# Kernel optimization log

Measured on AMD Instinct MI355X. Metric: run time of the kernel, lower is better.

## Reference

```python
import jax, jax.numpy as jnp
import numpy as np

DIMS = [1, 16, 32, 64, 128, 64, 32, 1]  # linear chain dims, LN+ReLU after first 6 linears
EPS = 1e-5  # torch LayerNorm default


def _ln(x, g, b):
    m = jnp.mean(x, axis=-1, keepdims=True)
    v = jnp.var(x, axis=-1, keepdims=True)  # biased var, matches torch LayerNorm
    return (x - m) * jax.lax.rsqrt(v + EPS) * g + b


def setup_inputs() -> dict:
    key = jax.random.key(0)
    N = 1_048_576
    keys = jax.random.split(key, 1 + 7 * 2)
    inp = {"x": jax.random.normal(keys[0], (N, 1), dtype=jnp.float32)}
    for i in range(7):
        fan_in, fan_out = DIMS[i], DIMS[i + 1]
        bound = 1.0 / np.sqrt(fan_in)
        inp[f"W{i}"] = jax.random.uniform(keys[1 + 2 * i], (fan_in, fan_out), jnp.float32, -bound, bound)
        inp[f"b{i}"] = jax.random.uniform(keys[2 + 2 * i], (fan_out,), jnp.float32, -bound, bound)
    for i in range(6):  # LayerNorm affine params (init: gamma=1, beta=0)
        inp[f"g{i}"] = jnp.ones((DIMS[i + 1],), jnp.float32)
        inp[f"be{i}"] = jnp.zeros((DIMS[i + 1],), jnp.float32)
    return inp


def reference(x, W0, W1, W2, W3, W4, W5, W6,
              b0, b1, b2, b3, b4, b5, b6,
              g0, g1, g2, g3, g4, g5,
              be0, be1, be2, be3, be4, be5):
    Ws = [W0, W1, W2, W3, W4, W5, W6]
    bs = [b0, b1, b2, b3, b4, b5, b6]
    gs = [g0, g1, g2, g3, g4, g5]
    bes = [be0, be1, be2, be3, be4, be5]
    h = x
    for i in range(7):
        h = h @ Ws[i] + bs[i]
        if i < 6:
            h = jax.nn.relu(_ln(h, gs[i], bes[i]))
    return h
```

## Files before the change

kernel.cpp:

```cpp
#include <hip/hip_runtime.h>
#include <math.h>

#define EPS_LN 1e-5f
#define TPTS 32768
#define BT 256
#define NBLK 256

constexpr int WS_CNT  = 0;
constexpr int WS_PART = 64;
constexpr int WS_MMF  = 640;
constexpr size_t WS_TABLE_OFF = 4096;

struct Params {
  const float *W0,*b0,*W1,*b1,*W2,*b2,*W3,*b3,*W4,*b4,*W5,*b5,*W6,*b6;
  const float *g0,*be0,*g1,*be1,*g2,*be2,*g3,*be3,*g4,*be4,*g5,*be5;
};

constexpr int O_W0 = 0;      constexpr int O_B0 = 16;
constexpr int O_W1 = 32;     constexpr int O_B1 = 544;
constexpr int O_W2 = 576;    constexpr int O_B2 = 2624;
constexpr int O_W3 = 2688;   constexpr int O_B3 = 10880;
constexpr int O_W4 = 11008;  constexpr int O_B4 = 19200;
constexpr int O_W5 = 19264;  constexpr int O_B5 = 21312;
constexpr int O_W6 = 21344;  constexpr int O_B6 = 21376;
constexpr int O_G0 = 21380;  constexpr int O_BE0 = 21396;
constexpr int O_G1 = 21412;  constexpr int O_BE1 = 21444;
constexpr int O_G2 = 21476;  constexpr int O_BE2 = 21540;
constexpr int O_G3 = 21604;  constexpr int O_BE3 = 21732;
constexpr int O_G4 = 21860;  constexpr int O_BE4 = 21924;
constexpr int O_G5 = 21988;  constexpr int O_BE5 = 22020;
constexpr int SMEM_FLOATS = 22052;

__device__ __forceinline__ unsigned enc_f(float f) {
  unsigned u = __float_as_uint(f);
  return (u & 0x80000000u) ? ~u : (u | 0x80000000u);
}
__device__ __forceinline__ float dec_f(unsigned k) {
  unsigned u = (k & 0x80000000u) ? (k ^ 0x80000000u) : ~k;
  return __uint_as_float(u);
}

__device__ __forceinline__ void stage(float* sm, int off, const float* __restrict__ src,
                                      int n, int t) {
  for (int i = t; i < n; i += BT) sm[off + i] = src[i];
}
template<int IN, int OUT>
__device__ __forceinline__ void stage_wP(float* sm, int off, const float* __restrict__ src,
                                         int t) {
  constexpr int U = OUT / 4, NC = OUT / 32;
  for (int u = t; u < IN * U; u += BT) {
    int i = u / U, d = u - i * U;
    int c = d >> 3, rr = d & 7;
    int s = rr * NC + c;
    *reinterpret_cast<float4*>(sm + off + i * OUT + d * 4) =
        *reinterpret_cast<const float4*>(src + i * OUT + s * 4);
  }
}

__device__ __forceinline__ void stage_all(float* sm, const Params& P, int t) {
  stage(sm, O_W0, P.W0, 16, t);         stage(sm, O_B0, P.b0, 16, t);
  stage_wP<16, 32>(sm, O_W1, P.W1, t);  stage(sm, O_B1, P.b1, 32, t);
  stage_wP<32, 64>(sm, O_W2, P.W2, t);  stage(sm, O_B2, P.b2, 64, t);
  stage_wP<64, 128>(sm, O_W3, P.W3, t); stage(sm, O_B3, P.b3, 128, t);
  stage_wP<128, 64>(sm, O_W4, P.W4, t); stage(sm, O_B4, P.b4, 64, t);
  stage_wP<64, 32>(sm, O_W5, P.W5, t);  stage(sm, O_B5, P.b5, 32, t);
  stage(sm, O_W6, P.W6, 32, t);         stage(sm, O_B6, P.b6, 1, t);
  stage(sm, O_G0, P.g0, 16, t);         stage(sm, O_BE0, P.be0, 16, t);
  stage(sm, O_G1, P.g1, 32, t);         stage(sm, O_BE1, P.be1, 32, t);
  stage(sm, O_G2, P.g2, 64, t);         stage(sm, O_BE2, P.be2, 64, t);
  stage(sm, O_G3, P.g3, 128, t);        stage(sm, O_BE3, P.be3, 128, t);
  stage(sm, O_G4, P.g4, 64, t);         stage(sm, O_BE4, P.be4, 64, t);
  stage(sm, O_G5, P.g5, 32, t);         stage(sm, O_BE5, P.be5, 32, t);
}

__device__ __forceinline__ float gred8(float v) {
  v += __shfl_xor(v, 1);
  v += __shfl_xor(v, 2);
  v += __shfl_xor(v, 4);
  return v;
}

template<int IN, int OUT>
__device__ __forceinline__ void lin8(const float (&ain)[4][IN / 8],
                                     float (&aout)[4][OUT / 8],
                                     const float* __restrict__ Ws,
                                     const float* __restrict__ bs, int r) {
  constexpr int INP = IN / 8, OUTP = OUT / 8, NC = OUTP / 4;
  #pragma unroll
  for (int c = 0; c < NC; ++c) {
    float4 b4 = *reinterpret_cast<const float4*>(bs + r * OUTP + c * 4);
    #pragma unroll
    for (int p = 0; p < 4; ++p) {
      aout[p][c * 4 + 0] = b4.x; aout[p][c * 4 + 1] = b4.y;
      aout[p][c * 4 + 2] = b4.z; aout[p][c * 4 + 3] = b4.w;
    }
  }
  #pragma unroll
  for (int i = 0; i < IN; ++i) {
    float vb[4];
    #pragma unroll
    for (int p = 0; p < 4; ++p) vb[p] = __shfl(ain[p][i % INP], i / INP, 8);
    #pragma unroll
    for (int c = 0; c < NC; ++c) {
      float4 w = *reinterpret_cast<const float4*>(Ws + i * OUT + (c * 8 + r) * 4);
      #pragma unroll
      for (int p = 0; p < 4; ++p) {
        aout[p][c * 4 + 0] = fmaf(vb[p], w.x, aout[p][c * 4 + 0]);
        aout[p][c * 4 + 1] = fmaf(vb[p], w.y, aout[p][c * 4 + 1]);
        aout[p][c * 4 + 2] = fmaf(vb[p], w.z, aout[p][c * 4 + 2]);
        aout[p][c * 4 + 3] = fmaf(vb[p], w.w, aout[p][c * 4 + 3]);
      }
    }
  }
}

template<int D>
__device__ __forceinline__ void ln8(float (&h)[4][D / 8],
                                    const float* __restrict__ g,
                                    const float* __restrict__ be, int r) {
  constexpr int DP = D / 8;
  float m[4], sc[4];
  #pragma unroll
  for (int p = 0; p < 4; ++p) {
    float s = 0.f;
    #pragma unroll
    for (int j = 0; j < DP; ++j) s += h[p][j];
    m[p] = gred8(s) * (1.0f / (float)D);
  }
  #pragma unroll
  for (int p = 0; p < 4; ++p) {
    float vs = 0.f;
    #pragma unroll
    for (int j = 0; j < DP; ++j) { float d = h[p][j] - m[p]; vs = fmaf(d, d, vs); }
    sc[p] = rsqrtf(gred8(vs) * (1.0f / (float)D) + EPS_LN);
  }
  #pragma unroll
  for (int j = 0; j < DP; ++j) {
    float gj = g[r * DP + j], bej = be[r * DP + j];
    #pragma unroll
    for (int p = 0; p < 4; ++p) {
      float tt = (h[p][j] - m[p]) * sc[p];
      tt = fmaf(tt, gj, bej);
      h[p][j] = fmaxf(tt, 0.0f);
    }
  }
}

__device__ __forceinline__ void eval8(const float (&xp)[4], int r,
                                      const float* __restrict__ sm, float (&y)[4]) {
  float a0[4][2];
  #pragma unroll
  for (int j = 0; j < 2; ++j) {
    float w = sm[O_W0 + r * 2 + j], bb = sm[O_B0 + r * 2 + j];
    #pragma unroll
    for (int p = 0; p < 4; ++p) a0[p][j] = fmaf(xp[p], w, bb);
  }
  ln8<16>(a0, sm + O_G0, sm + O_BE0, r);
  float a1[4][4];  lin8<16, 32>(a0, a1, sm + O_W1, sm + O_B1, r);  ln8<32>(a1, sm + O_G1, sm + O_BE1, r);
  float a2[4][8];  lin8<32, 64>(a1, a2, sm + O_W2, sm + O_B2, r);  ln8<64>(a2, sm + O_G2, sm + O_BE2, r);
  float a3[4][16]; lin8<64, 128>(a2, a3, sm + O_W3, sm + O_B3, r); ln8<128>(a3, sm + O_G3, sm + O_BE3, r);
  float a4[4][8];  lin8<128, 64>(a3, a4, sm + O_W4, sm + O_B4, r); ln8<64>(a4, sm + O_G4, sm + O_BE4, r);
  float a5[4][4];  lin8<64, 32>(a4, a5, sm + O_W5, sm + O_B5, r);  ln8<32>(a5, sm + O_G5, sm + O_BE5, r);
  float4 wv = *reinterpret_cast<const float4*>(sm + O_W6 + r * 4);
  #pragma unroll
  for (int p = 0; p < 4; ++p) {
    float d = a5[p][0] * wv.x;
    d = fmaf(a5[p][1], wv.y, d);
    d = fmaf(a5[p][2], wv.z, d);
    d = fmaf(a5[p][3], wv.w, d);
    y[p] = gred8(d) + sm[O_B6];
  }
}

__device__ __forceinline__ void range_from_keys(unsigned kmin, unsigned kmax,
                                                float& lo, float& step, float& istep) {
  float fmin = dec_f(kmin) - 1e-3f;
  float fmax = dec_f(kmax) + 1e-3f;
  lo = fmin;
  float span = fmax - fmin;
  step  = span * (1.0f / (float)(TPTS - 1));
  istep = (float)(TPTS - 1) / span;
}

__global__ __launch_bounds__(BT)
__attribute__((amdgpu_waves_per_eu(1, 1)))
void fused_kernel(const float* __restrict__ x, int n,
                  unsigned* __restrict__ wsu, float* __restrict__ table,
                  Params P) {
  __shared__ float sm[SMEM_FLOATS];
  __shared__ float redmn[4], redmx[4];
  __shared__ unsigned redk[8];
  const int t = threadIdx.x;
  const int b = blockIdx.x;

  stage_all(sm, P, t);

  const int gtid = b * BT + t;
  const int gstride = NBLK * BT;
  float lmin = 3.0e38f, lmax = -3.0e38f;
  for (int i = gtid * 4; i + 3 < n; i += gstride * 4) {
    float4 v = *reinterpret_cast<const float4*>(x + i);
    lmin = fminf(lmin, fminf(fminf(v.x, v.y), fminf(v.z, v.w)));
    lmax = fmaxf(lmax, fmaxf(fmaxf(v.x, v.y), fmaxf(v.z, v.w)));
  }
  if (gtid == 0) {
    for (int i = n & ~3; i < n; ++i) { lmin = fminf(lmin, x[i]); lmax = fmaxf(lmax, x[i]); }
  }
  #pragma unroll
  for (int off = 32; off > 0; off >>= 1) {
    lmin = fminf(lmin, __shfl_xor(lmin, off));
    lmax = fmaxf(lmax, __shfl_xor(lmax, off));
  }
  if ((t & 63) == 0) { redmn[t >> 6] = lmin; redmx[t >> 6] = lmax; }
  __syncthreads();

  if (t == 0) {
    float bmin = redmn[0], bmax = redmx[0];
    #pragma unroll
    for (int w = 1; w < 4; ++w) { bmin = fminf(bmin, redmn[w]); bmax = fmaxf(bmax, redmx[w]); }
    __hip_atomic_store(&wsu[WS_PART + 2 * b],     enc_f(bmin),
                       __ATOMIC_RELEASE, __HIP_MEMORY_SCOPE_AGENT);
    __hip_atomic_store(&wsu[WS_PART + 2 * b + 1], enc_f(bmax),
                       __ATOMIC_RELEASE, __HIP_MEMORY_SCOPE_AGENT);
    __hip_atomic_fetch_add(&wsu[WS_CNT], 1u, __ATOMIC_ACQ_REL, __HIP_MEMORY_SCOPE_AGENT);
    while (__hip_atomic_load(&wsu[WS_CNT], __ATOMIC_ACQUIRE, __HIP_MEMORY_SCOPE_AGENT) < NBLK)
      __builtin_amdgcn_s_sleep(8);
  }
  __syncthreads();

  {
    unsigned kmin = __hip_atomic_load(&wsu[WS_PART + 2 * t], __ATOMIC_RELAXED,
                                      __HIP_MEMORY_SCOPE_AGENT);
    unsigned kmax = __hip_atomic_load(&wsu[WS_PART + 2 * t + 1], __ATOMIC_RELAXED,
                                      __HIP_MEMORY_SCOPE_AGENT);
    #pragma unroll
    for (int off = 32; off > 0; off >>= 1) {
      kmin = min(kmin, (unsigned)__shfl_xor((int)kmin, off));
      kmax = max(kmax, (unsigned)__shfl_xor((int)kmax, off));
    }
    if ((t & 63) == 0) { redk[t >> 6] = kmin; redk[4 + (t >> 6)] = kmax; }
  }
  __syncthreads();
  unsigned ukmin = redk[0], ukmax = redk[4];
  #pragma unroll
  for (int w = 1; w < 4; ++w) { ukmin = min(ukmin, redk[w]); ukmax = max(ukmax, redk[4 + w]); }
  if (b == 0 && t == 0) { wsu[WS_MMF] = ukmin; wsu[WS_MMF + 1] = ukmax; }

  float lo, step, istep;
  range_from_keys(ukmin, ukmax, lo, step, istep);
  const int r = t & 7;
  const int base = b * 128 + (t >> 3) * 4;
  float xp[4], y[4];
  #pragma unroll
  for (int p = 0; p < 4; ++p) xp[p] = fmaf((float)(base + p), step, lo);
  eval8(xp, r, sm, y);
  if (r == 0)
    *reinterpret_cast<float4*>(table + base) = make_float4(y[0], y[1], y[2], y[3]);
}

__device__ __forceinline__ float interp_lds(float xv, float lo, float istep,
                                            const float* __restrict__ tl) {
  float tt = (xv - lo) * istep;
  tt = fminf(fmaxf(tt, 0.0f), (float)(TPTS - 1));
  int i = (int)tt;
  if (i > TPTS - 2) i = TPTS - 2;
  float f = tt - (float)i;
  float t0 = tl[i], t1 = tl[i + 1];
  return fmaf(f, t1 - t0, t0);
}

__global__ __launch_bounds__(256) void lookup_kernel(const float* __restrict__ x,
                                                     const float* __restrict__ table,
                                                     const unsigned* __restrict__ wsu,
                                                     float* __restrict__ out, int n) {
  __shared__ float tl[TPTS];
  for (int i = threadIdx.x; i < TPTS / 4; i += 256)
    reinterpret_cast<float4*>(tl)[i] = reinterpret_cast<const float4*>(table)[i];
  float lo, step, istep;
  range_from_keys(wsu[WS_MMF], wsu[WS_MMF + 1], lo, step, istep);
  __syncthreads();

  int tid = blockIdx.x * blockDim.x + threadIdx.x;
  int stride = gridDim.x * blockDim.x;
  for (int i = tid * 4; i + 3 < n; i += stride * 4) {
    float4 v = *reinterpret_cast<const float4*>(x + i);
    float4 rr;
    rr.x = interp_lds(v.x, lo, istep, tl);
    rr.y = interp_lds(v.y, lo, istep, tl);
    rr.z = interp_lds(v.z, lo, istep, tl);
    rr.w = interp_lds(v.w, lo, istep, tl);
    *reinterpret_cast<float4*>(out + i) = rr;
  }
  if (tid == 0) {
    for (int i = n & ~3; i < n; ++i) out[i] = interp_lds(x[i], lo, istep, tl);
  }
}

__global__ __launch_bounds__(BT)
__attribute__((amdgpu_waves_per_eu(1, 1)))
void direct_kernel(const float* __restrict__ x, float* __restrict__ out, int n,
                   Params P) {
  __shared__ float sm[SMEM_FLOATS];
  const int t = threadIdx.x;
  stage_all(sm, P, t);
  __syncthreads();
  const int r = t & 7;
  const int gstride = gridDim.x * (BT / 8) * 4;
  for (int base = (blockIdx.x * (BT / 8) + (t >> 3)) * 4; base < n; base += gstride) {
    float xp[4], y[4];
    #pragma unroll
    for (int p = 0; p < 4; ++p) xp[p] = (base + p < n) ? x[base + p] : 0.0f;
    eval8(xp, r, sm, y);
    if (r == 0) {
      #pragma unroll
      for (int p = 0; p < 4; ++p) if (base + p < n) out[base + p] = y[p];
    }
  }
}

extern "C" void kernel_launch(void* const* d_in, const int* in_sizes, int n_in,
                              void* d_out, int out_size, void* d_ws, size_t ws_size,
                              hipStream_t stream) {
  const float* x = (const float*)d_in[0];
  Params P;
  P.W0 = (const float*)d_in[1];  P.b0 = (const float*)d_in[2];
  P.W1 = (const float*)d_in[3];  P.b1 = (const float*)d_in[4];
  P.W2 = (const float*)d_in[5];  P.b2 = (const float*)d_in[6];
  P.W3 = (const float*)d_in[7];  P.b3 = (const float*)d_in[8];
  P.W4 = (const float*)d_in[9];  P.b4 = (const float*)d_in[10];
  P.W5 = (const float*)d_in[11]; P.b5 = (const float*)d_in[12];
  P.W6 = (const float*)d_in[13]; P.b6 = (const float*)d_in[14];
  P.g0 = (const float*)d_in[15]; P.be0 = (const float*)d_in[16];
  P.g1 = (const float*)d_in[17]; P.be1 = (const float*)d_in[18];
  P.g2 = (const float*)d_in[19]; P.be2 = (const float*)d_in[20];
  P.g3 = (const float*)d_in[21]; P.be3 = (const float*)d_in[22];
  P.g4 = (const float*)d_in[23]; P.be4 = (const float*)d_in[24];
  P.g5 = (const float*)d_in[25]; P.be5 = (const float*)d_in[26];

  int n = in_sizes[0];
  float* out = (float*)d_out;

  if (ws_size < WS_TABLE_OFF + (size_t)TPTS * sizeof(float)) {
    direct_kernel<<<NBLK, BT, 0, stream>>>(x, out, n, P);
    return;
  }

  unsigned* wsu = (unsigned*)d_ws;
  float* table = (float*)((char*)d_ws + WS_TABLE_OFF);

  hipMemsetAsync(d_ws, 0, 64, stream);
  fused_kernel<<<NBLK, BT, 0, stream>>>(x, n, wsu, table, P);
  lookup_kernel<<<256, 256, 0, stream>>>(x, table, wsu, out, n);
}
```

Measured before the change: 172.6 us.

## Gather lookup table from global memory and reshape fused grid to 128x512

The lookup kernel no longer stages the 128 KB interpolation table into LDS in every block. It gathers table entries straight from global memory (through L2), and its grid grows from 256 to 1024 blocks. The fused table-building kernel now runs 128 blocks of 512 threads instead of 256 of 256, and its reduction and table-index arithmetic are adjusted to match. This removes the per-block LDS fill and the occupancy limit it imposed, at the cost of scattered global loads for each interpolation.

New measurement: 242.7 us. +40.6%, slower.

```diff
diff --git a/kernel.cpp b/kernel.cpp
--- a/kernel.cpp
+++ b/kernel.cpp
@@ -3,8 +3,8 @@
 
 #define EPS_LN 1e-5f
 #define TPTS 32768
-#define BT 256
-#define NBLK 256
+#define BT 512
+#define NBLK 128
 
 constexpr int WS_CNT  = 0;
 constexpr int WS_PART = 64;
@@ -183,13 +183,13 @@
 }
 
 __global__ __launch_bounds__(BT)
-__attribute__((amdgpu_waves_per_eu(1, 1)))
+__attribute__((amdgpu_waves_per_eu(2, 2)))
 void fused_kernel(const float* __restrict__ x, int n,
                   unsigned* __restrict__ wsu, float* __restrict__ table,
                   Params P) {
   __shared__ float sm[SMEM_FLOATS];
-  __shared__ float redmn[4], redmx[4];
-  __shared__ unsigned redk[8];
+  __shared__ float redmn[8], redmx[8];
+  __shared__ unsigned redk[16];
   const int t = threadIdx.x;
   const int b = blockIdx.x;
 
@@ -217,7 +217,7 @@
   if (t == 0) {
     float bmin = redmn[0], bmax = redmx[0];
     #pragma unroll
-    for (int w = 1; w < 4; ++w) { bmin = fminf(bmin, redmn[w]); bmax = fmaxf(bmax, redmx[w]); }
+    for (int w = 1; w < 8; ++w) { bmin = fminf(bmin, redmn[w]); bmax = fmaxf(bmax, redmx[w]); }
     __hip_atomic_store(&wsu[WS_PART + 2 * b],     enc_f(bmin),
                        __ATOMIC_RELEASE, __HIP_MEMORY_SCOPE_AGENT);
     __hip_atomic_store(&wsu[WS_PART + 2 * b + 1], enc_f(bmax),
@@ -229,27 +229,29 @@
   __syncthreads();
 
   {
-    unsigned kmin = __hip_atomic_load(&wsu[WS_PART + 2 * t], __ATOMIC_RELAXED,
-                                      __HIP_MEMORY_SCOPE_AGENT);
-    unsigned kmax = __hip_atomic_load(&wsu[WS_PART + 2 * t + 1], __ATOMIC_RELAXED,
-                                      __HIP_MEMORY_SCOPE_AGENT);
+    unsigned kmin = 0xFFFFFFFFu, kmax = 0u;
+    if (t < NBLK) {
+      kmin = __hip_atomic_load(&wsu[WS_PART + 2 * t], __ATOMIC_RELAXED,
+                               __HIP_MEMORY_SCOPE_AGENT);
+      kmax = __hip_atomic_load(&wsu[WS_PART + 2 * t + 1], __ATOMIC_RELAXED,
+                               __HIP_MEMORY_SCOPE_AGENT);
+    }
     #pragma unroll
     for (int off = 32; off > 0; off >>= 1) {
       kmin = min(kmin, (unsigned)__shfl_xor((int)kmin, off));
       kmax = max(kmax, (unsigned)__shfl_xor((int)kmax, off));
     }
-    if ((t & 63) == 0) { redk[t >> 6] = kmin; redk[4 + (t >> 6)] = kmax; }
+    if ((t & 63) == 0 && t < NBLK) { redk[t >> 6] = kmin; redk[8 + (t >> 6)] = kmax; }
   }
   __syncthreads();
-  unsigned ukmin = redk[0], ukmax = redk[4];
-  #pragma unroll
-  for (int w = 1; w < 4; ++w) { ukmin = min(ukmin, redk[w]); ukmax = max(ukmax, redk[4 + w]); }
+  unsigned ukmin = min(redk[0], redk[1]);
+  unsigned ukmax = max(redk[8], redk[9]);
   if (b == 0 && t == 0) { wsu[WS_MMF] = ukmin; wsu[WS_MMF + 1] = ukmax; }
 
   float lo, step, istep;
   range_from_keys(ukmin, ukmax, lo, step, istep);
   const int r = t & 7;
-  const int base = b * 128 + (t >> 3) * 4;
+  const int base = b * 256 + (t >> 3) * 4;
   float xp[4], y[4];
   #pragma unroll
   for (int p = 0; p < 4; ++p) xp[p] = fmaf((float)(base + p), step, lo);
@@ -258,14 +260,14 @@
     *reinterpret_cast<float4*>(table + base) = make_float4(y[0], y[1], y[2], y[3]);
 }
 
-__device__ __forceinline__ float interp_lds(float xv, float lo, float istep,
-                                            const float* __restrict__ tl) {
+__device__ __forceinline__ float interp(float xv, float lo, float istep,
+                                        const float* __restrict__ tb) {
   float tt = (xv - lo) * istep;
   tt = fminf(fmaxf(tt, 0.0f), (float)(TPTS - 1));
   int i = (int)tt;
   if (i > TPTS - 2) i = TPTS - 2;
   float f = tt - (float)i;
-  float t0 = tl[i], t1 = tl[i + 1];
+  float t0 = tb[i], t1 = tb[i + 1];
   return fmaf(f, t1 - t0, t0);
 }
 
@@ -273,31 +275,26 @@
                                                      const float* __restrict__ table,
                                                      const unsigned* __restrict__ wsu,
                                                      float* __restrict__ out, int n) {
-  __shared__ float tl[TPTS];
-  for (int i = threadIdx.x; i < TPTS / 4; i += 256)
-    reinterpret_cast<float4*>(tl)[i] = reinterpret_cast<const float4*>(table)[i];
   float lo, step, istep;
   range_from_keys(wsu[WS_MMF], wsu[WS_MMF + 1], lo, step, istep);
-  __syncthreads();
-
   int tid = blockIdx.x * blockDim.x + threadIdx.x;
   int stride = gridDim.x * blockDim.x;
   for (int i = tid * 4; i + 3 < n; i += stride * 4) {
     float4 v = *reinterpret_cast<const float4*>(x + i);
     float4 rr;
-    rr.x = interp_lds(v.x, lo, istep, tl);
-    rr.y = interp_lds(v.y, lo, istep, tl);
-    rr.z = interp_lds(v.z, lo, istep, tl);
-    rr.w = interp_lds(v.w, lo, istep, tl);
+    rr.x = interp(v.x, lo, istep, table);
+    rr.y = interp(v.y, lo, istep, table);
+    rr.z = interp(v.z, lo, istep, table);
+    rr.w = interp(v.w, lo, istep, table);
     *reinterpret_cast<float4*>(out + i) = rr;
   }
   if (tid == 0) {
-    for (int i = n & ~3; i < n; ++i) out[i] = interp_lds(x[i], lo, istep, tl);
+    for (int i = n & ~3; i < n; ++i) out[i] = interp(x[i], lo, istep, table);
   }
 }
 
 __global__ __launch_bounds__(BT)
-__attribute__((amdgpu_waves_per_eu(1, 1)))
+__attribute__((amdgpu_waves_per_eu(2, 2)))
 void direct_kernel(const float* __restrict__ x, float* __restrict__ out, int n,
                    Params P) {
   __shared__ float sm[SMEM_FLOATS];
@@ -341,7 +338,7 @@
   float* out = (float*)d_out;
 
   if (ws_size < WS_TABLE_OFF + (size_t)TPTS * sizeof(float)) {
-    direct_kernel<<<NBLK, BT, 0, stream>>>(x, out, n, P);
+    direct_kernel<<<256, BT, 0, stream>>>(x, out, n, P);
     return;
   }
 
@@ -350,5 +347,5 @@
 
   hipMemsetAsync(d_ws, 0, 64, stream);
   fused_kernel<<<NBLK, BT, 0, stream>>>(x, n, wsu, table, P);
-  lookup_kernel<<<256, 256, 0, stream>>>(x, table, wsu, out, n);
-}
+  lookup_kernel<<<1024, 256, 0, stream>>>(x, table, wsu, out, n);
+}
```
